# Kernel tuning notes

Measured on AMD Instinct MI355X. Metric: run time of the kernel, lower is better.

Reference implementation:

```python
import jax, jax.numpy as jnp
import numpy as np

def setup_inputs() -> dict:
    key = jax.random.key(0)
    kq, kk, kv = jax.random.split(key, 3)
    B, H, N, D = 2, 12, 4096, 64
    Q = jax.random.normal(kq, (B, H, N, D), dtype=jnp.float32)
    K = jax.random.normal(kk, (B, H, N, D), dtype=jnp.float32)
    V = jax.random.normal(kv, (B, H, N, D), dtype=jnp.float32)
    mask = jnp.ones((B, N), dtype=jnp.float32)
    return {"Q": Q, "K": K, "V": V, "mask": mask}

def reference(Q, K, V, mask):
    # Q, K, V: [B, H, N, D]; mask: [B, N]
    N = Q.shape[2]
    scale = 1.0 / jnp.sqrt(jnp.sqrt(jnp.float32(N)))  # N^(-1/4)
    m = mask[:, None, :, None]                         # [B,1,N,1]
    Qf = (jax.nn.elu(Q) + 1.0) * scale                 # feature map on queries
    Kf = (jax.nn.elu(K) + 1.0) * m * scale             # feature map + mask on keys
    Vm = V * m
    # linear attention: Q (K^T V), contracting over sequence first -> [B,H,D,D]
    KtV = jnp.einsum('bhnd,bhne->bhde', Kf, Vm)
    X = jnp.einsum('bhnd,bhde->bhne', Qf, KtV)
    return X
```

## Files before the change

kernel.cpp:

```cpp
#include <hip/hip_runtime.h>
#include <hip/hip_bf16.h>
#include <math.h>


#define BH_TOT 24
#define NROWS 4096
#define DD 64

typedef __attribute__((ext_vector_type(8))) short bf16x8;
typedef __attribute__((ext_vector_type(4))) float f32x4;

__device__ __forceinline__ float elu1(float x) {
    return x > 0.0f ? x + 1.0f : __expf(x);
}
__device__ __forceinline__ short f2bf(float x) {
    __hip_bfloat16 h = __float2bfloat16(x);
    return *reinterpret_cast<short*>(&h);
}

__global__ __launch_bounds__(256) void la_pass1(
        const float* __restrict__ K, const float* __restrict__ V,
        const float* __restrict__ mask, float* __restrict__ partial,
        float scale, int chunksPerWave) {
    const int bh   = blockIdx.x;
    const int wave = threadIdx.x >> 6;
    const int lane = threadIdx.x & 63;
    const int widx = blockIdx.y * 4 + wave;
    const int rg   = (lane >> 4) * 8;
    const int cl   = lane & 15;

    const float* __restrict__ Kp = K + (size_t)bh * NROWS * DD;
    const float* __restrict__ Vp = V + (size_t)bh * NROWS * DD;
    const float* __restrict__ mp = mask + (size_t)(bh / 12) * NROWS;

    f32x4 acc[4][4];
#pragma unroll
    for (int i = 0; i < 4; ++i)
#pragma unroll
        for (int j = 0; j < 4; ++j) acc[i][j] = (f32x4)0.0f;

    const int n0 = widx * chunksPerWave * 32;

#pragma unroll 1
    for (int c = 0; c < chunksPerWave; ++c) {
        const int nb = n0 + c * 32 + rg;
        const float* kb = Kp + (size_t)nb * DD + cl;
        const float* vb = Vp + (size_t)nb * DD + cl;
        float mrow[8], kr[8][4], vr[8][4];
#pragma unroll
        for (int jj = 0; jj < 8; ++jj) {
            mrow[jj] = mp[nb + jj];
#pragma unroll
            for (int i = 0; i < 4; ++i) {
                kr[jj][i] = kb[jj * DD + i * 16];
                vr[jj][i] = vb[jj * DD + i * 16];
            }
        }
        bf16x8 af[4], bf[4];
#pragma unroll
        for (int i = 0; i < 4; ++i)
#pragma unroll
            for (int jj = 0; jj < 8; ++jj) {
                af[i][jj] = f2bf(elu1(kr[jj][i]) * (mrow[jj] * scale));
                bf[i][jj] = f2bf(vr[jj][i] * mrow[jj]);
            }
#pragma unroll
        for (int i = 0; i < 4; ++i)
#pragma unroll
            for (int j = 0; j < 4; ++j)
                acc[i][j] = __builtin_amdgcn_mfma_f32_16x16x32_bf16(
                                af[i], bf[j], acc[i][j], 0, 0, 0);
    }

    float* out = partial + ((size_t)bh * gridDim.y * 4 + widx) * (DD * DD);
#pragma unroll
    for (int i = 0; i < 4; ++i)
#pragma unroll
        for (int j = 0; j < 4; ++j)
#pragma unroll
            for (int r = 0; r < 4; ++r)
                out[(16 * i + (lane >> 4) * 4 + r) * DD + 16 * j + cl] = acc[i][j][r];
}

__global__ __launch_bounds__(256) void la_pass2(
        const float* __restrict__ partial, __hip_bfloat16* __restrict__ ktvT,
        int nw) {
    const int bh = blockIdx.x;
    const int f4 = blockIdx.y * 256 + threadIdx.x;
    const f32x4* base = (const f32x4*)(partial + (size_t)bh * nw * DD * DD) + f4;
    f32x4 s = (f32x4)0.0f;
#pragma unroll 8
    for (int w = 0; w < nw; ++w)
        s += base[(size_t)w * (DD * DD / 4)];
    const int d = f4 >> 4, e0 = (f4 & 15) * 4;
    __hip_bfloat16* o = ktvT + (size_t)bh * DD * DD + d;
#pragma unroll
    for (int q = 0; q < 4; ++q)
        o[(size_t)(e0 + q) * DD] = __float2bfloat16(s[q]);
}

__global__ __launch_bounds__(256) void la_pass3(
        const float* __restrict__ Q, const __hip_bfloat16* __restrict__ ktvT,
        float* __restrict__ X, float scale) {
    const int bh   = blockIdx.x;
    const int wave = threadIdx.x >> 6;
    const int lane = threadIdx.x & 63;
    const int n0   = blockIdx.y * 128 + wave * 32;
    const int rg   = (lane >> 4) * 8;
    const int cl   = lane & 15;

    bf16x8 bfr[2][4];
#pragma unroll
    for (int c2 = 0; c2 < 2; ++c2)
#pragma unroll
        for (int j = 0; j < 4; ++j) {
            const __hip_bfloat16* p = ktvT + (size_t)bh * DD * DD
                                      + (size_t)(16 * j + cl) * DD + 32 * c2 + rg;
            bfr[c2][j] = *reinterpret_cast<const bf16x8*>(p);
        }

    const float* Qp = Q + (size_t)bh * NROWS * DD;
    bf16x8 afr[2][2];
#pragma unroll
    for (int i = 0; i < 2; ++i)
#pragma unroll
        for (int c2 = 0; c2 < 2; ++c2) {
            const float* qp = Qp + (size_t)(n0 + 16 * i + cl) * DD + 32 * c2 + rg;
            float4 q0 = ((const float4*)qp)[0];
            float4 q1 = ((const float4*)qp)[1];
            bf16x8 a;
            a[0] = f2bf(elu1(q0.x) * scale); a[1] = f2bf(elu1(q0.y) * scale);
            a[2] = f2bf(elu1(q0.z) * scale); a[3] = f2bf(elu1(q0.w) * scale);
            a[4] = f2bf(elu1(q1.x) * scale); a[5] = f2bf(elu1(q1.y) * scale);
            a[6] = f2bf(elu1(q1.z) * scale); a[7] = f2bf(elu1(q1.w) * scale);
            afr[i][c2] = a;
        }

    f32x4 acc[2][4];
#pragma unroll
    for (int i = 0; i < 2; ++i)
#pragma unroll
        for (int j = 0; j < 4; ++j) acc[i][j] = (f32x4)0.0f;

#pragma unroll
    for (int i = 0; i < 2; ++i)
#pragma unroll
        for (int j = 0; j < 4; ++j) {
            acc[i][j] = __builtin_amdgcn_mfma_f32_16x16x32_bf16(
                            afr[i][0], bfr[0][j], acc[i][j], 0, 0, 0);
            acc[i][j] = __builtin_amdgcn_mfma_f32_16x16x32_bf16(
                            afr[i][1], bfr[1][j], acc[i][j], 0, 0, 0);
        }

    float* Xp = X + (size_t)bh * NROWS * DD;
#pragma unroll
    for (int i = 0; i < 2; ++i)
#pragma unroll
        for (int j = 0; j < 4; ++j)
#pragma unroll
            for (int r = 0; r < 4; ++r)
                Xp[(size_t)(n0 + 16 * i + (lane >> 4) * 4 + r) * DD + 16 * j + cl]
                    = acc[i][j][r];
}

extern "C" void kernel_launch(void* const* d_in, const int* in_sizes, int n_in,
                              void* d_out, int out_size, void* d_ws, size_t ws_size,
                              hipStream_t stream) {
    const float* Q    = (const float*)d_in[0];
    const float* K    = (const float*)d_in[1];
    const float* V    = (const float*)d_in[2];
    const float* mask = (const float*)d_in[3];
    float* X = (float*)d_out;

    const float scale = 0.125f;

    int nw = 64;
    while (nw > 4 &&
           (size_t)BH_TOT * nw * DD * DD * 4 + (size_t)BH_TOT * DD * DD * 2 > ws_size)
        nw >>= 1;
    const int chunksPerWave = NROWS / (nw * 32);

    float* partial = (float*)d_ws;
    __hip_bfloat16* ktvT =
        (__hip_bfloat16*)((char*)d_ws + (size_t)BH_TOT * nw * DD * DD * 4);

    la_pass1<<<dim3(BH_TOT, nw / 4), 256, 0, stream>>>(K, V, mask, partial,
                                                       scale, chunksPerWave);
    la_pass2<<<dim3(BH_TOT, 4), 256, 0, stream>>>(partial, ktvT, nw);
    la_pass3<<<dim3(BH_TOT, 32), 256, 0, stream>>>(Q, ktvT, X, scale);
}
```

Before: 36.99 us.

## Reduce per-wave KtV partials in shared memory before writing to global

Each pass1 block now combines the four per-wave 64x64 partial accumulators in LDS with a two-step tree reduction and writes a single partial per block. This cuts the number of partials per head from up to 64 to 16, reducing global writes in pass1 and reads in pass2. It adds LDS usage (about 33KB per block) and extra barriers, and removes the workspace-size fallback.

```diff
diff --git a/kernel.cpp b/kernel.cpp
--- a/kernel.cpp
+++ b/kernel.cpp
@@ -6,6 +6,7 @@
 #define BH_TOT 24
 #define NROWS 4096
 #define DD 64
+#define NB 16
 
 typedef __attribute__((ext_vector_type(8))) short bf16x8;
 typedef __attribute__((ext_vector_type(4))) float f32x4;
@@ -23,10 +24,11 @@
         const float* __restrict__ mask, float* __restrict__ partial,
         float scale, int chunksPerWave) {
     const int bh   = blockIdx.x;
+    const int blk  = blockIdx.y;
     const int wave = threadIdx.x >> 6;
     const int lane = threadIdx.x & 63;
-    const int widx = blockIdx.y * 4 + wave;
-    const int rg   = (lane >> 4) * 8;
+    const int g    = lane >> 4;
+    const int rg   = g * 8;
     const int cl   = lane & 15;
 
     const float* __restrict__ Kp = K + (size_t)bh * NROWS * DD;
@@ -39,7 +41,7 @@
 #pragma unroll
         for (int j = 0; j < 4; ++j) acc[i][j] = (f32x4)0.0f;
 
-    const int n0 = widx * chunksPerWave * 32;
+    const int n0 = (blk * 4 + wave) * chunksPerWave * 32;
 
 #pragma unroll 1
     for (int c = 0; c < chunksPerWave; ++c) {
@@ -56,30 +58,67 @@
                 vr[jj][i] = vb[jj * DD + i * 16];
             }
         }
-        bf16x8 af[4], bf[4];
+        bf16x8 af[4], bfv[4];
 #pragma unroll
         for (int i = 0; i < 4; ++i)
 #pragma unroll
             for (int jj = 0; jj < 8; ++jj) {
-                af[i][jj] = f2bf(elu1(kr[jj][i]) * (mrow[jj] * scale));
-                bf[i][jj] = f2bf(vr[jj][i] * mrow[jj]);
+                af[i][jj]  = f2bf(elu1(kr[jj][i]) * (mrow[jj] * scale));
+                bfv[i][jj] = f2bf(vr[jj][i] * mrow[jj]);
             }
 #pragma unroll
         for (int i = 0; i < 4; ++i)
 #pragma unroll
             for (int j = 0; j < 4; ++j)
                 acc[i][j] = __builtin_amdgcn_mfma_f32_16x16x32_bf16(
-                                af[i], bf[j], acc[i][j], 0, 0, 0);
-    }
-
-    float* out = partial + ((size_t)bh * gridDim.y * 4 + widx) * (DD * DD);
-#pragma unroll
-    for (int i = 0; i < 4; ++i)
-#pragma unroll
-        for (int j = 0; j < 4; ++j)
-#pragma unroll
-            for (int r = 0; r < 4; ++r)
-                out[(16 * i + (lane >> 4) * 4 + r) * DD + 16 * j + cl] = acc[i][j][r];
+                                af[i], bfv[j], acc[i][j], 0, 0, 0);
+    }
+
+    __shared__ float red[2][DD * 66];
+#define RIDX(i, r, j) ((16 * (i) + 4 * g + (r)) * 66 + 16 * (j) + cl)
+    if (wave >= 2) {
+        float* buf = red[wave - 2];
+#pragma unroll
+        for (int i = 0; i < 4; ++i)
+#pragma unroll
+            for (int j = 0; j < 4; ++j)
+#pragma unroll
+                for (int r = 0; r < 4; ++r) buf[RIDX(i, r, j)] = acc[i][j][r];
+    }
+    __syncthreads();
+    if (wave < 2) {
+        const float* buf = red[wave];
+#pragma unroll
+        for (int i = 0; i < 4; ++i)
+#pragma unroll
+            for (int j = 0; j < 4; ++j)
+#pragma unroll
+                for (int r = 0; r < 4; ++r) acc[i][j][r] += buf[RIDX(i, r, j)];
+    }
+    __syncthreads();
+    if (wave == 1) {
+        float* buf = red[0];
+#pragma unroll
+        for (int i = 0; i < 4; ++i)
+#pragma unroll
+            for (int j = 0; j < 4; ++j)
+#pragma unroll
+                for (int r = 0; r < 4; ++r) buf[RIDX(i, r, j)] = acc[i][j][r];
+    }
+    __syncthreads();
+    if (wave == 0) {
+        const float* buf = red[0];
+        float* out = partial + ((size_t)bh * NB + blk) * (DD * DD);
+#pragma unroll
+        for (int i = 0; i < 4; ++i)
+#pragma unroll
+            for (int j = 0; j < 4; ++j)
+#pragma unroll
+                for (int r = 0; r < 4; ++r)
+                    out[(16 * i + 4 * g + r) * DD + 16 * j + cl]
+                        = acc[i][j][r] + buf[RIDX(i, r, j)];
+    }
+#undef RIDX
 }
 
 __global__ __launch_bounds__(256) void la_pass2(
@@ -174,18 +213,14 @@
 
     const float scale = 0.125f;
 
-    int nw = 64;
-    while (nw > 4 &&
-           (size_t)BH_TOT * nw * DD * DD * 4 + (size_t)BH_TOT * DD * DD * 2 > ws_size)
-        nw >>= 1;
-    const int chunksPerWave = NROWS / (nw * 32);
+    const int chunksPerWave = NROWS / (NB * 4 * 32);
 
     float* partial = (float*)d_ws;
     __hip_bfloat16* ktvT =
-        (__hip_bfloat16*)((char*)d_ws + (size_t)BH_TOT * nw * DD * DD * 4);
-
-    la_pass1<<<dim3(BH_TOT, nw / 4), 256, 0, stream>>>(K, V, mask, partial,
-                                                       scale, chunksPerWave);
-    la_pass2<<<dim3(BH_TOT, 4), 256, 0, stream>>>(partial, ktvT, nw);
+        (__hip_bfloat16*)((char*)d_ws + (size_t)BH_TOT * NB * DD * DD * 4);
+
+    la_pass1<<<dim3(BH_TOT, NB), 256, 0, stream>>>(K, V, mask, partial,
+                                                   scale, chunksPerWave);
+    la_pass2<<<dim3(BH_TOT, 4), 256, 0, stream>>>(partial, ktvT, NB);
     la_pass3<<<dim3(BH_TOT, 32), 256, 0, stream>>>(Q, ktvT, X, scale);
 }
```

Measured after the change: 32.88 us. 11.1% less time.

## Reduce pass1 partials in LDS across two waves before writing to workspace

Applied to the files above, without the earlier changes.

Pass1 now launches 128-thread blocks of two waves. The second wave hands its 64x64 KtV partial to the first wave through shared memory, and the first wave adds it to its own and writes a single partial per block. This halves the number of partial matrices written to global memory and read back by the pass2 reduction. In exchange it adds an LDS round trip, a block barrier, and about 16.5 KB of shared memory per block.

```diff
diff --git a/kernel.cpp b/kernel.cpp
--- a/kernel.cpp
+++ b/kernel.cpp
@@ -18,16 +18,15 @@
     return *reinterpret_cast<short*>(&h);
 }
 
-__global__ __launch_bounds__(256) void la_pass1(
+__global__ __launch_bounds__(128) void la_pass1(
         const float* __restrict__ K, const float* __restrict__ V,
         const float* __restrict__ mask, float* __restrict__ partial,
         float scale, int chunksPerWave) {
     const int bh   = blockIdx.x;
+    const int slab = blockIdx.y;
     const int wave = threadIdx.x >> 6;
     const int lane = threadIdx.x & 63;
-    const int widx = blockIdx.y * 4 + wave;
-    const int rg   = (lane >> 4) * 8;
-    const int cl   = lane & 15;
+    const int g = lane >> 4, rg = g * 8, cl = lane & 15;
 
     const float* __restrict__ Kp = K + (size_t)bh * NROWS * DD;
     const float* __restrict__ Vp = V + (size_t)bh * NROWS * DD;
@@ -39,7 +38,8 @@
 #pragma unroll
         for (int j = 0; j < 4; ++j) acc[i][j] = (f32x4)0.0f;
 
-    const int n0 = widx * chunksPerWave * 32;
+    const int rowsPerBlock = chunksPerWave * 64;
+    const int n0 = slab * rowsPerBlock + wave * chunksPerWave * 32;
 
 #pragma unroll 1
     for (int c = 0; c < chunksPerWave; ++c) {
@@ -56,30 +56,45 @@
                 vr[jj][i] = vb[jj * DD + i * 16];
             }
         }
-        bf16x8 af[4], bf[4];
+        bf16x8 af[4], bv[4];
 #pragma unroll
         for (int i = 0; i < 4; ++i)
 #pragma unroll
             for (int jj = 0; jj < 8; ++jj) {
                 af[i][jj] = f2bf(elu1(kr[jj][i]) * (mrow[jj] * scale));
-                bf[i][jj] = f2bf(vr[jj][i] * mrow[jj]);
+                bv[i][jj] = f2bf(vr[jj][i] * mrow[jj]);
             }
 #pragma unroll
         for (int i = 0; i < 4; ++i)
 #pragma unroll
             for (int j = 0; j < 4; ++j)
                 acc[i][j] = __builtin_amdgcn_mfma_f32_16x16x32_bf16(
-                                af[i], bf[j], acc[i][j], 0, 0, 0);
+                                af[i], bv[j], acc[i][j], 0, 0, 0);
     }
 
-    float* out = partial + ((size_t)bh * gridDim.y * 4 + widx) * (DD * DD);
-#pragma unroll
-    for (int i = 0; i < 4; ++i)
-#pragma unroll
-        for (int j = 0; j < 4; ++j)
-#pragma unroll
-            for (int r = 0; r < 4; ++r)
-                out[(16 * i + (lane >> 4) * 4 + r) * DD + 16 * j + cl] = acc[i][j][r];
+    __shared__ float red[DD * 66];
+#define RIDX(i, r, j) ((16 * (i) + 4 * g + (r)) * 66 + 16 * (j) + cl)
+    if (wave == 1) {
+#pragma unroll
+        for (int i = 0; i < 4; ++i)
+#pragma unroll
+            for (int j = 0; j < 4; ++j)
+#pragma unroll
+                for (int r = 0; r < 4; ++r) red[RIDX(i, r, j)] = acc[i][j][r];
+    }
+    __syncthreads();
+    if (wave == 0) {
+        float* out = partial + ((size_t)bh * gridDim.y + slab) * (DD * DD);
+#pragma unroll
+        for (int i = 0; i < 4; ++i)
+#pragma unroll
+            for (int j = 0; j < 4; ++j)
+#pragma unroll
+                for (int r = 0; r < 4; ++r)
+                    out[(16 * i + 4 * g + r) * DD + 16 * j + cl]
+                        = acc[i][j][r] + red[RIDX(i, r, j)];
+    }
+#undef RIDX
 }
 
 __global__ __launch_bounds__(256) void la_pass2(
@@ -174,18 +189,18 @@
 
     const float scale = 0.125f;
 
-    int nw = 64;
-    while (nw > 4 &&
-           (size_t)BH_TOT * nw * DD * DD * 4 + (size_t)BH_TOT * DD * DD * 2 > ws_size)
-        nw >>= 1;
-    const int chunksPerWave = NROWS / (nw * 32);
+    int slabs = 32;
+    while (slabs > 4 &&
+           (size_t)BH_TOT * slabs * DD * DD * 4 + (size_t)BH_TOT * DD * DD * 2 > ws_size)
+        slabs >>= 1;
+    const int chunksPerWave = NROWS / (slabs * 64);
 
     float* partial = (float*)d_ws;
     __hip_bfloat16* ktvT =
-        (__hip_bfloat16*)((char*)d_ws + (size_t)BH_TOT * nw * DD * DD * 4);
-
-    la_pass1<<<dim3(BH_TOT, nw / 4), 256, 0, stream>>>(K, V, mask, partial,
-                                                       scale, chunksPerWave);
-    la_pass2<<<dim3(BH_TOT, 4), 256, 0, stream>>>(partial, ktvT, nw);
+        (__hip_bfloat16*)((char*)d_ws + (size_t)BH_TOT * slabs * DD * DD * 4);
+
+    la_pass1<<<dim3(BH_TOT, slabs), 128, 0, stream>>>(K, V, mask, partial,
+                                                      scale, chunksPerWave);
+    la_pass2<<<dim3(BH_TOT, 4), 256, 0, stream>>>(partial, ktvT, slabs);
     la_pass3<<<dim3(BH_TOT, 32), 256, 0, stream>>>(Q, ktvT, X, scale);
 }
```

After: 34.23 us. -7.5%, faster.
